# Optimization experiments

Hardware: AMD Instinct MI355X
Metric: run time of the kernel (lower is better)

The kernel has to match this reference:

```python
import jax, jax.numpy as jnp
import numpy as np

IN_C = 512
OUT_C = 1024
N = 8192


def _xavier(key, shape):
    fan_in, fan_out = shape[1], shape[0]
    limit = float(np.sqrt(6.0 / (fan_in + fan_out)))
    return jax.random.uniform(key, shape, jnp.float32, -limit, limit)


def setup_inputs() -> dict:
    key = jax.random.key(0)
    ks = jax.random.split(key, 20)
    inp = {
        'x': jax.random.normal(ks[0], (IN_C, N), jnp.float32),
        'c_prev_dim0': jax.random.normal(ks[1], (OUT_C, N), jnp.float32),
        'h_prev_dim0': jax.random.normal(ks[2], (OUT_C, N), jnp.float32),
        'c_prev_dim1': jax.random.normal(ks[3], (OUT_C, N), jnp.float32),
        'h_prev_dim1': jax.random.normal(ks[4], (OUT_C, N), jnp.float32),
    }
    names_x = ['w_ii', 'w_if', 'w_ig', 'w_io']
    names_h = ['w_hi', 'w_hf', 'w_hg', 'w_ho']
    names_b = ['b_i', 'b_f', 'b_g', 'b_o']
    k = 5
    for n in names_x:
        inp[n] = _xavier(ks[k], (OUT_C, IN_C)); k += 1
    for n in names_h:
        inp[n] = _xavier(ks[k], (OUT_C, OUT_C)); k += 1
    for n in names_b:
        inp[n] = _xavier(ks[k], (OUT_C, 1)); k += 1
    inp['weighted_sum'] = jax.random.uniform(ks[k], (2,), jnp.float32)
    return inp


def reference(x, c_prev_dim0, h_prev_dim0, c_prev_dim1, h_prev_dim1,
              w_ii, w_if, w_ig, w_io,
              w_hi, w_hf, w_hg, w_ho,
              b_i, b_f, b_g, b_o,
              weighted_sum):
    # Input projections shared by both spatial directions: (out, N)
    xi = w_ii @ x
    xf = w_if @ x
    xg = w_ig @ x
    xo = w_io @ x

    def gates(h_prev, c_prev):
        i = jax.nn.sigmoid(xi + w_hi @ h_prev + b_i)
        f = jax.nn.sigmoid(xf + w_hf @ h_prev + b_f)
        g = jnp.tanh(xg + w_hg @ h_prev + b_g)
        o = jax.nn.sigmoid(xo + w_ho @ h_prev + b_o)
        c = f * c_prev + i * g
        h = o * jnp.tanh(c)
        return c, h

    ct0, ht0 = gates(h_prev_dim0, c_prev_dim0)
    ct1, ht1 = gates(h_prev_dim1, c_prev_dim1)
    ct = ct0 * weighted_sum[0] + ct1 * weighted_sum[1]
    ht = ht0 * weighted_sum[0] + ht1 * weighted_sum[1]
    return ct, ht
```

## Files before the change

kernel.cpp:

```cpp
#include <hip/hip_runtime.h>
#include <cstdint>
#include <cstddef>

#define IN_C  512
#define OUT_C 1024
#define NSAMP 8192
#define KTOT  1536

typedef __bf16 bf16x8 __attribute__((ext_vector_type(8)));
typedef float  f32x4  __attribute__((ext_vector_type(4)));

#define SBAR()   __builtin_amdgcn_s_barrier()
#define SFENCE() __builtin_amdgcn_sched_barrier(0)
#define VM4()    asm volatile("s_waitcnt vmcnt(4)")
#define VM0()    asm volatile("s_waitcnt vmcnt(0)")

__device__ __forceinline__ unsigned short f2bf(float f) {
    unsigned int u = __float_as_uint(f);
    u += 0x7FFFu + ((u >> 16) & 1u);
    return (unsigned short)(u >> 16);
}
__device__ __forceinline__ float sigmoid_f(float x) { return 1.0f / (1.0f + __expf(-x)); }
__device__ __forceinline__ float tanh_f(float x) {
    float e = __expf(2.0f * x);
    return 1.0f - 2.0f / (e + 1.0f);
}

__global__ void tcvt_kernel(const float* __restrict__ in, unsigned short* __restrict__ out,
                            int R, int C) {
    __shared__ float t[32][33];
    const int tx = threadIdx.x, ty = threadIdx.y;
    const int c0 = blockIdx.x * 32, r0 = blockIdx.y * 32;
#pragma unroll
    for (int i = 0; i < 4; ++i)
        t[ty + i * 8][tx] = in[(size_t)(r0 + ty + i * 8) * C + (c0 + tx)];
    __syncthreads();
#pragma unroll
    for (int i = 0; i < 4; ++i)
        out[(size_t)(c0 + ty + i * 8) * R + (r0 + tx)] = f2bf(t[tx][ty + i * 8]);
}

__global__ void packA_kernel(const float* __restrict__ x0, const float* __restrict__ x1,
                             const float* __restrict__ x2, const float* __restrict__ x3,
                             const float* __restrict__ h0, const float* __restrict__ h1,
                             const float* __restrict__ h2, const float* __restrict__ h3,
                             unsigned short* __restrict__ Ap) {
    const int idx = blockIdx.x * 256 + threadIdx.x;
    const int m = idx / 192, k8 = idx % 192;
    const int g = m & 3, r = m >> 2;
    const float* src;
    if (k8 < 64) {
        const float* a = (g & 2) ? ((g & 1) ? x3 : x2) : ((g & 1) ? x1 : x0);
        src = a + (size_t)r * IN_C + k8 * 8;
    } else {
        const float* a = (g & 2) ? ((g & 1) ? h3 : h2) : ((g & 1) ? h1 : h0);
        src = a + (size_t)r * OUT_C + (k8 - 64) * 8;
    }
    float4 v0 = reinterpret_cast<const float4*>(src)[0];
    float4 v1 = reinterpret_cast<const float4*>(src)[1];
    ushort4 o0, o1;
    o0.x = f2bf(v0.x); o0.y = f2bf(v0.y); o0.z = f2bf(v0.z); o0.w = f2bf(v0.w);
    o1.x = f2bf(v1.x); o1.y = f2bf(v1.y); o1.z = f2bf(v1.z); o1.w = f2bf(v1.w);
    ushort4* dst = reinterpret_cast<ushort4*>(Ap + (size_t)m * KTOT + k8 * 8);
    dst[0] = o0; dst[1] = o1;
}

__global__ __launch_bounds__(512, 2) void mdlstm_main(
    const unsigned short* __restrict__ Ap,
    const unsigned short* __restrict__ xT,
    const unsigned short* __restrict__ h0T,
    const unsigned short* __restrict__ h1T,
    const float* __restrict__ b_i, const float* __restrict__ b_f,
    const float* __restrict__ b_g, const float* __restrict__ b_o,
    const float* __restrict__ cp0, const float* __restrict__ cp1,
    const float* __restrict__ wsum,
    float* __restrict__ out)
{
    __shared__ __align__(16) unsigned char smem[131072];

    const int tid  = threadIdx.x;
    const int lane = tid & 63;
    const int wid  = tid >> 6;
    const int wm   = wid >> 2;
    const int wn   = wid & 3;
    const int g4   = lane >> 4;
    const int l16  = lane & 15;

    const int by    = blockIdx.y;
    const int bcol  = blockIdx.x * 128;
    const int browM = by * 256;

    f32x4 acc[8][4];
#pragma unroll
    for (int mf = 0; mf < 8; ++mf)
#pragma unroll
        for (int nf = 0; nf < 4; ++nf)
            acc[mf][nf] = (f32x4){0.f, 0.f, 0.f, 0.f};

    auto stage_A = [&](int P, int hA, int j1) {
#pragma unroll
        for (int c = 0; c < 2; ++c) {
            const int u    = c * 8192 + tid * 16;
            const int rloc = (u >> 6) & 127;
            const int kb   = (u & 63) ^ (((u >> 7) & 3) << 4);
            const char* src = (const char*)Ap
                + ((size_t)(browM + hA * 128 + rloc) * KTOT + j1 * 64 + c * 32) * 2 + kb;
            __builtin_amdgcn_global_load_lds((const unsigned int*)src,
                (unsigned int*)(smem + P * 65536 + hA * 16384 + u), 16, 0, 0);
        }
    };
    auto stage_B = [&](int P, int d, int j2) {
#pragma unroll
        for (int c = 0; c < 2; ++c) {
            const int u    = c * 8192 + tid * 16;
            const int rloc = (u >> 6) & 127;
            const int kb   = (u & 63) ^ (((u >> 7) & 3) << 4);
            const char* src;
            if (j2 < 8) {
                src = (const char*)xT + ((size_t)(bcol + rloc) * IN_C + j2 * 64 + c * 32) * 2 + kb;
            } else {
                const unsigned short* hsrc = d ? h1T : h0T;
                src = (const char*)hsrc + ((size_t)(bcol + rloc) * OUT_C + (j2 - 8) * 64 + c * 32) * 2 + kb;
            }
            __builtin_amdgcn_global_load_lds((const unsigned int*)src,
                (unsigned int*)(smem + P * 65536 + 32768 + d * 16384 + u), 16, 0, 0);
        }
    };

    auto swzb = [](int u) { return u ^ (((u >> 7) & 3) << 4); };
    auto fragA = [&](int P, int mf, int kk) -> bf16x8 {
        const int u = kk * 8192 + (mf * 16 + l16) * 64 + g4 * 16;
        return *reinterpret_cast<const bf16x8*>(smem + P * 65536 + wm * 16384 + swzb(u));
    };
    auto fragB = [&](int P, int nf, int kk) -> bf16x8 {
        const int u = kk * 8192 + ((wn & 1) * 64 + nf * 16 + l16) * 64 + g4 * 16;
        return *reinterpret_cast<const bf16x8*>(smem + P * 65536 + 32768 + (wn >> 1) * 16384 + swzb(u));
    };

    bf16x8 aF[2][2];
    bf16x8 bF[4][2];

    auto cluster = [&](int M) {
        __builtin_amdgcn_s_setprio(1);
#pragma unroll
        for (int kk = 0; kk < 2; ++kk)
#pragma unroll
            for (int mi = 0; mi < 2; ++mi)
#pragma unroll
                for (int nf = 0; nf < 4; ++nf)
                    acc[M + mi][nf] = __builtin_amdgcn_mfma_f32_16x16x32_bf16(
                        aF[mi][kk], bF[nf][kk], acc[M + mi][nf], 0, 0, 0);
        __builtin_amdgcn_s_setprio(0);
    };
    auto loadA = [&](int P, int mf) {
#pragma unroll
        for (int kk = 0; kk < 2; ++kk) { aF[0][kk] = fragA(P, mf, kk); aF[1][kk] = fragA(P, mf + 1, kk); }
    };
    auto loadB = [&](int P) {
#pragma unroll
        for (int nf = 0; nf < 4; ++nf)
#pragma unroll
            for (int kk = 0; kk < 2; ++kk) bF[nf][kk] = fragB(P, nf, kk);
    };

    auto ktile = [&](int j, int P, int PN) {
        const bool stA = (j < 23);
        const bool stB = (j < 22);
        cluster(0);
        loadA(P, 2);
        if (stA) stage_A(PN, 0, j + 1);
        SBAR();
        cluster(2);
        loadA(P, 4);
        if (stA) stage_A(PN, 1, j + 1);
        SBAR();
        cluster(4);
        loadA(P, 6);
        if (stB) stage_B(P, 0, j + 2);
        SBAR();
        cluster(6);
        if (stB) stage_B(P, 1, j + 2);
        if (j < 22)       { SFENCE(); VM4(); SFENCE(); }
        else if (j == 22) { SFENCE(); VM0(); SFENCE(); }
        if (j < 23) { loadB(PN); loadA(PN, 0); }
        SBAR();
    };

    stage_A(0, 0, 0); stage_A(0, 1, 0);
    stage_B(0, 0, 0); stage_B(0, 1, 0);
    stage_B(1, 0, 1); stage_B(1, 1, 1);
    SFENCE(); VM4(); SFENCE();
    SBAR();
    loadB(0); loadA(0, 0);

#pragma unroll 1
    for (int jj = 0; jj < 12; ++jj) {
        ktile(2 * jj,     0, 1);
        ktile(2 * jj + 1, 1, 0);
    }

    const float w0 = wsum[0], w1 = wsum[1];
    const int   d  = wn >> 1;
    const float* cp = d ? cp1 : cp0;
    const float wd  = d ? w1 : w0;

    float rc[8][4], rh[8][4];
#pragma unroll
    for (int mf = 0; mf < 8; ++mf) {
        const int orow = by * 64 + wm * 32 + mf * 4 + g4;
        const float bi = b_i[orow], bff = b_f[orow], bg = b_g[orow], bo = b_o[orow];
#pragma unroll
        for (int nf = 0; nf < 4; ++nf) {
            const int scol = bcol + (wn & 1) * 64 + nf * 16 + l16;
            float i_ = sigmoid_f(acc[mf][nf][0] + bi);
            float f_ = sigmoid_f(acc[mf][nf][1] + bff);
            float g_ = tanh_f  (acc[mf][nf][2] + bg);
            float o_ = sigmoid_f(acc[mf][nf][3] + bo);
            float cc = f_ * cp[(size_t)orow * NSAMP + scol] + i_ * g_;
            float hh = o_ * tanh_f(cc);
            rc[mf][nf] = wd * cc;
            rh[mf][nf] = wd * hh;
        }
    }

    float* ex = (float*)smem;
    const int rbase = (wm * 2 + (wn & 1)) * 4096;
    if (d == 1) {
#pragma unroll
        for (int mf = 0; mf < 8; ++mf)
#pragma unroll
            for (int nf = 0; nf < 4; ++nf) {
                const int slot = rbase + (mf * 4 + nf) * 64 + lane;
                ex[slot]        = rc[mf][nf];
                ex[slot + 2048] = rh[mf][nf];
            }
    }
    SBAR();
    if (d == 0) {
#pragma unroll
        for (int mf = 0; mf < 8; ++mf) {
            const int orow = by * 64 + wm * 32 + mf * 4 + g4;
#pragma unroll
            for (int nf = 0; nf < 4; ++nf) {
                const int scol = bcol + (wn & 1) * 64 + nf * 16 + l16;
                const int slot = rbase + (mf * 4 + nf) * 64 + lane;
                out[(size_t)orow * NSAMP + scol] = rc[mf][nf] + ex[slot];
                out[(size_t)OUT_C * NSAMP + (size_t)orow * NSAMP + scol] = rh[mf][nf] + ex[slot + 2048];
            }
        }
    }
}

extern "C" void kernel_launch(void* const* d_in, const int* in_sizes, int n_in,
                              void* d_out, int out_size, void* d_ws, size_t ws_size,
                              hipStream_t stream) {
    (void)in_sizes; (void)n_in; (void)out_size; (void)ws_size;

    const float* x    = (const float*)d_in[0];
    const float* cp0  = (const float*)d_in[1];
    const float* hp0  = (const float*)d_in[2];
    const float* cp1  = (const float*)d_in[3];
    const float* hp1  = (const float*)d_in[4];
    const float* b_i  = (const float*)d_in[13];
    const float* b_f  = (const float*)d_in[14];
    const float* b_g  = (const float*)d_in[15];
    const float* b_o  = (const float*)d_in[16];
    const float* wsum = (const float*)d_in[17];
    float* out = (float*)d_out;

    char* ws = (char*)d_ws;
    unsigned short* xT  = (unsigned short*)(ws);
    unsigned short* h0T = (unsigned short*)(ws + (size_t)8  * 1024 * 1024);
    unsigned short* h1T = (unsigned short*)(ws + (size_t)24 * 1024 * 1024);
    unsigned short* Ap  = (unsigned short*)(ws + (size_t)40 * 1024 * 1024);

    dim3 tb(32, 8);
    tcvt_kernel<<<dim3(NSAMP / 32, IN_C  / 32), tb, 0, stream>>>(x,   xT,  IN_C,  NSAMP);
    tcvt_kernel<<<dim3(NSAMP / 32, OUT_C / 32), tb, 0, stream>>>(hp0, h0T, OUT_C, NSAMP);
    tcvt_kernel<<<dim3(NSAMP / 32, OUT_C / 32), tb, 0, stream>>>(hp1, h1T, OUT_C, NSAMP);

    packA_kernel<<<(4096 * 192) / 256, 256, 0, stream>>>(
        (const float*)d_in[5], (const float*)d_in[6], (const float*)d_in[7], (const float*)d_in[8],
        (const float*)d_in[9], (const float*)d_in[10], (const float*)d_in[11], (const float*)d_in[12],
        Ap);

    mdlstm_main<<<dim3(NSAMP / 128, OUT_C / 64), 512, 0, stream>>>(
        Ap, xT, h0T, h1T, b_i, b_f, b_g, b_o, cp0, cp1, wsum, out);
}
```

Measured before the change: 245.7 us.

## Switch GEMM inner loop to 32x32x16 MFMA with two-phase k-tile schedule

Replaces the 16x16x32 bf16 MFMA tiles with 32x32x16 instructions. Each wave now holds four by two 32x32 accumulator blocks, and the fragment reads, swizzle and epilogue index mapping are rewritten to match. The k-tile loop is restructured from four interleaved clusters with prefetched fragments into two phases: load fragments, issue the staging copies, barrier, then compute. The larger MFMA reduces LDS fragment traffic per flop and the instruction count, at the cost of less overlap between LDS reads and MFMA issue within a k-tile.

```diff
diff --git a/kernel.cpp b/kernel.cpp
--- a/kernel.cpp
+++ b/kernel.cpp
@@ -8,7 +8,7 @@
 #define KTOT  1536
 
 typedef __bf16 bf16x8 __attribute__((ext_vector_type(8)));
-typedef float  f32x4  __attribute__((ext_vector_type(4)));
+typedef float  f32x16 __attribute__((ext_vector_type(16)));
 
 #define SBAR()   __builtin_amdgcn_s_barrier()
 #define SFENCE() __builtin_amdgcn_sched_barrier(0)
@@ -83,19 +83,21 @@
     const int wid  = tid >> 6;
     const int wm   = wid >> 2;
     const int wn   = wid & 3;
-    const int g4   = lane >> 4;
-    const int l16  = lane & 15;
+    const int l31  = lane & 31;
+    const int h32  = lane >> 5;
 
     const int by    = blockIdx.y;
     const int bcol  = blockIdx.x * 128;
     const int browM = by * 256;
 
-    f32x4 acc[8][4];
-#pragma unroll
-    for (int mf = 0; mf < 8; ++mf)
-#pragma unroll
-        for (int nf = 0; nf < 4; ++nf)
-            acc[mf][nf] = (f32x4){0.f, 0.f, 0.f, 0.f};
+    f32x16 acc[4][2];
+#pragma unroll
+    for (int mb = 0; mb < 4; ++mb)
+#pragma unroll
+        for (int nb = 0; nb < 2; ++nb)
+#pragma unroll
+            for (int r = 0; r < 16; ++r)
+                acc[mb][nb][r] = 0.f;
 
     auto stage_A = [&](int P, int hA, int j1) {
 #pragma unroll
@@ -127,62 +129,63 @@
         }
     };
 
-    auto swzb = [](int u) { return u ^ (((u >> 7) & 3) << 4); };
-    auto fragA = [&](int P, int mf, int kk) -> bf16x8 {
-        const int u = kk * 8192 + (mf * 16 + l16) * 64 + g4 * 16;
-        return *reinterpret_cast<const bf16x8*>(smem + P * 65536 + wm * 16384 + swzb(u));
-    };
-    auto fragB = [&](int P, int nf, int kk) -> bf16x8 {
-        const int u = kk * 8192 + ((wn & 1) * 64 + nf * 16 + l16) * 64 + g4 * 16;
-        return *reinterpret_cast<const bf16x8*>(smem + P * 65536 + 32768 + (wn >> 1) * 16384 + swzb(u));
-    };
-
-    bf16x8 aF[2][2];
-    bf16x8 bF[4][2];
-
-    auto cluster = [&](int M) {
+    auto fragA = [&](int P, int mb, int s) -> bf16x8 {
+        const int rloc = mb * 32 + l31;
+        const int u = (s >> 1) * 8192 + rloc * 64
+                    + (((s & 1) * 32 + h32 * 16) ^ (((rloc >> 1) & 3) << 4));
+        return *reinterpret_cast<const bf16x8*>(smem + P * 65536 + wm * 16384 + u);
+    };
+    auto fragB = [&](int P, int nb, int s) -> bf16x8 {
+        const int rloc = (wn & 1) * 64 + nb * 32 + l31;
+        const int u = (s >> 1) * 8192 + rloc * 64
+                    + (((s & 1) * 32 + h32 * 16) ^ (((rloc >> 1) & 3) << 4));
+        return *reinterpret_cast<const bf16x8*>(smem + P * 65536 + 32768 + (wn >> 1) * 16384 + u);
+    };
+
+    auto ktile = [&](int j, int P, int PN) {
+        const bool stA = (j < 23), stB = (j < 22);
+        bf16x8 aF[2][4], bF[2][4];
+
+#pragma unroll
+        for (int nb = 0; nb < 2; ++nb)
+#pragma unroll
+            for (int s = 0; s < 4; ++s) bF[nb][s] = fragB(P, nb, s);
+#pragma unroll
+        for (int mb = 0; mb < 2; ++mb)
+#pragma unroll
+            for (int s = 0; s < 4; ++s) aF[mb][s] = fragA(P, mb, s);
+        if (stA) { stage_A(PN, 0, j + 1); stage_A(PN, 1, j + 1); }
+        SBAR();
         __builtin_amdgcn_s_setprio(1);
 #pragma unroll
-        for (int kk = 0; kk < 2; ++kk)
-#pragma unroll
-            for (int mi = 0; mi < 2; ++mi)
-#pragma unroll
-                for (int nf = 0; nf < 4; ++nf)
-                    acc[M + mi][nf] = __builtin_amdgcn_mfma_f32_16x16x32_bf16(
-                        aF[mi][kk], bF[nf][kk], acc[M + mi][nf], 0, 0, 0);
+        for (int s = 0; s < 4; ++s)
+#pragma unroll
+            for (int mb = 0; mb < 2; ++mb)
+#pragma unroll
+                for (int nb = 0; nb < 2; ++nb)
+                    acc[mb][nb] = __builtin_amdgcn_mfma_f32_32x32x16_bf16(
+                        aF[mb][s], bF[nb][s], acc[mb][nb], 0, 0, 0);
         __builtin_amdgcn_s_setprio(0);
-    };
-    auto loadA = [&](int P, int mf) {
-#pragma unroll
-        for (int kk = 0; kk < 2; ++kk) { aF[0][kk] = fragA(P, mf, kk); aF[1][kk] = fragA(P, mf + 1, kk); }
-    };
-    auto loadB = [&](int P) {
-#pragma unroll
-        for (int nf = 0; nf < 4; ++nf)
-#pragma unroll
-            for (int kk = 0; kk < 2; ++kk) bF[nf][kk] = fragB(P, nf, kk);
-    };
-
-    auto ktile = [&](int j, int P, int PN) {
-        const bool stA = (j < 23);
-        const bool stB = (j < 22);
-        cluster(0);
-        loadA(P, 2);
-        if (stA) stage_A(PN, 0, j + 1);
-        SBAR();
-        cluster(2);
-        loadA(P, 4);
-        if (stA) stage_A(PN, 1, j + 1);
-        SBAR();
-        cluster(4);
-        loadA(P, 6);
-        if (stB) stage_B(P, 0, j + 2);
-        SBAR();
-        cluster(6);
-        if (stB) stage_B(P, 1, j + 2);
+        SBAR();
+
+#pragma unroll
+        for (int mb = 0; mb < 2; ++mb)
+#pragma unroll
+            for (int s = 0; s < 4; ++s) aF[mb][s] = fragA(P, mb + 2, s);
+        if (stB) { stage_B(P, 0, j + 2); stage_B(P, 1, j + 2); }
+        SBAR();
+        __builtin_amdgcn_s_setprio(1);
+#pragma unroll
+        for (int s = 0; s < 4; ++s)
+#pragma unroll
+            for (int mb = 0; mb < 2; ++mb)
+#pragma unroll
+                for (int nb = 0; nb < 2; ++nb)
+                    acc[mb + 2][nb] = __builtin_amdgcn_mfma_f32_32x32x16_bf16(
+                        aF[mb][s], bF[nb][s], acc[mb + 2][nb], 0, 0, 0);
+        __builtin_amdgcn_s_setprio(0);
         if (j < 22)       { SFENCE(); VM4(); SFENCE(); }
         else if (j == 22) { SFENCE(); VM0(); SFENCE(); }
-        if (j < 23) { loadB(PN); loadA(PN, 0); }
         SBAR();
     };
 
@@ -191,7 +194,6 @@
     stage_B(1, 0, 1); stage_B(1, 1, 1);
     SFENCE(); VM4(); SFENCE();
     SBAR();
-    loadB(0); loadA(0, 0);
 
 #pragma unroll 1
     for (int jj = 0; jj < 12; ++jj) {
@@ -199,55 +201,58 @@
         ktile(2 * jj + 1, 1, 0);
     }
 
-    const float w0 = wsum[0], w1 = wsum[1];
     const int   d  = wn >> 1;
     const float* cp = d ? cp1 : cp0;
-    const float wd  = d ? w1 : w0;
-
-    float rc[8][4], rh[8][4];
-#pragma unroll
-    for (int mf = 0; mf < 8; ++mf) {
-        const int orow = by * 64 + wm * 32 + mf * 4 + g4;
-        const float bi = b_i[orow], bff = b_f[orow], bg = b_g[orow], bo = b_o[orow];
-#pragma unroll
-        for (int nf = 0; nf < 4; ++nf) {
-            const int scol = bcol + (wn & 1) * 64 + nf * 16 + l16;
-            float i_ = sigmoid_f(acc[mf][nf][0] + bi);
-            float f_ = sigmoid_f(acc[mf][nf][1] + bff);
-            float g_ = tanh_f  (acc[mf][nf][2] + bg);
-            float o_ = sigmoid_f(acc[mf][nf][3] + bo);
-            float cc = f_ * cp[(size_t)orow * NSAMP + scol] + i_ * g_;
-            float hh = o_ * tanh_f(cc);
-            rc[mf][nf] = wd * cc;
-            rh[mf][nf] = wd * hh;
-        }
-    }
+    const float wd  = wsum[d];
+
+    float rc[4][2][4], rh[4][2][4];
+#pragma unroll
+    for (int mb = 0; mb < 4; ++mb)
+#pragma unroll
+        for (int nb = 0; nb < 2; ++nb)
+#pragma unroll
+            for (int q = 0; q < 4; ++q) {
+                const int orow = by * 64 + wm * 32 + mb * 8 + 2 * q + h32;
+                const int scol = bcol + (wn & 1) * 64 + nb * 32 + l31;
+                float i_ = sigmoid_f(acc[mb][nb][4 * q + 0] + b_i[orow]);
+                float f_ = sigmoid_f(acc[mb][nb][4 * q + 1] + b_f[orow]);
+                float g_ = tanh_f  (acc[mb][nb][4 * q + 2] + b_g[orow]);
+                float o_ = sigmoid_f(acc[mb][nb][4 * q + 3] + b_o[orow]);
+                float cc = f_ * cp[(size_t)orow * NSAMP + scol] + i_ * g_;
+                float hh = o_ * tanh_f(cc);
+                rc[mb][nb][q] = wd * cc;
+                rh[mb][nb][q] = wd * hh;
+            }
 
     float* ex = (float*)smem;
     const int rbase = (wm * 2 + (wn & 1)) * 4096;
     if (d == 1) {
 #pragma unroll
-        for (int mf = 0; mf < 8; ++mf)
-#pragma unroll
-            for (int nf = 0; nf < 4; ++nf) {
-                const int slot = rbase + (mf * 4 + nf) * 64 + lane;
-                ex[slot]        = rc[mf][nf];
-                ex[slot + 2048] = rh[mf][nf];
-            }
+        for (int mb = 0; mb < 4; ++mb)
+#pragma unroll
+            for (int nb = 0; nb < 2; ++nb)
+#pragma unroll
+                for (int q = 0; q < 4; ++q) {
+                    const int slot = rbase + ((mb * 2 + nb) * 4 + q) * 64 + lane;
+                    ex[slot]        = rc[mb][nb][q];
+                    ex[slot + 2048] = rh[mb][nb][q];
+                }
     }
     SBAR();
     if (d == 0) {
 #pragma unroll
-        for (int mf = 0; mf < 8; ++mf) {
-            const int orow = by * 64 + wm * 32 + mf * 4 + g4;
-#pragma unroll
-            for (int nf = 0; nf < 4; ++nf) {
-                const int scol = bcol + (wn & 1) * 64 + nf * 16 + l16;
-                const int slot = rbase + (mf * 4 + nf) * 64 + lane;
-                out[(size_t)orow * NSAMP + scol] = rc[mf][nf] + ex[slot];
-                out[(size_t)OUT_C * NSAMP + (size_t)orow * NSAMP + scol] = rh[mf][nf] + ex[slot + 2048];
-            }
-        }
+        for (int mb = 0; mb < 4; ++mb)
+#pragma unroll
+            for (int nb = 0; nb < 2; ++nb)
+#pragma unroll
+                for (int q = 0; q < 4; ++q) {
+                    const int orow = by * 64 + wm * 32 + mb * 8 + 2 * q + h32;
+                    const int scol = bcol + (wn & 1) * 64 + nb * 32 + l31;
+                    const int slot = rbase + ((mb * 2 + nb) * 4 + q) * 64 + lane;
+                    out[(size_t)orow * NSAMP + scol] = rc[mb][nb][q] + ex[slot];
+                    out[(size_t)OUT_C * NSAMP + (size_t)orow * NSAMP + scol]
+                        = rh[mb][nb][q] + ex[slot + 2048];
+                }
     }
 }
 
```

After: 274.4 us. 1.12x slower.
